# Kernel tuning notes

Measured on AMD Instinct MI355X. Metric: run time of the kernel, lower is better.

Reference implementation:

```python
import jax, jax.numpy as jnp
import numpy as np
import math

B, S, H = 2, 4096, 768
NH, HD = 12, 64  # num heads, head dim


def setup_inputs() -> dict:
    key = jax.random.key(0)
    ks = jax.random.split(key, 4)
    scale = 1.0 / math.sqrt(H)
    return {
        "hidden_states": jax.random.normal(ks[0], (B, S, H), jnp.float32),
        "attention_mask": jnp.zeros((B, 1, 1, S), jnp.float32),
        "Wq": jax.random.normal(ks[1], (H, H), jnp.float32) * scale,
        "bq": jnp.zeros((H,), jnp.float32),
        "Wk": jax.random.normal(ks[2], (H, H), jnp.float32) * scale,
        "bk": jnp.zeros((H,), jnp.float32),
        "Wv": jax.random.normal(ks[3], (H, H), jnp.float32) * scale,
        "bv": jnp.zeros((H,), jnp.float32),
    }


def reference(hidden_states, attention_mask, Wq, bq, Wk, bk, Wv, bv):
    # Linear projections (torch nn.Linear: x @ W.T + b)
    q = hidden_states @ Wq.T + bq  # [B,S,H]
    k = hidden_states @ Wk.T + bk
    v = hidden_states @ Wv.T + bv
    # split heads -> [B, NH, S, HD]
    def split(x):
        return x.reshape(B, S, NH, HD).transpose(0, 2, 1, 3)
    qh, kh, vh = split(q), split(k), split(v)
    scores = jnp.einsum('bhqd,bhkd->bhqk', qh, kh) / math.sqrt(HD)
    scores = scores + attention_mask  # additive mask, broadcast
    probs = jax.nn.softmax(scores, axis=-1)
    # dropout prob = 0.0 (inference) -> identity
    ctx = jnp.einsum('bhqk,bhkd->bhqd', probs, vh)
    ctx = ctx.transpose(0, 2, 1, 3).reshape(B, S, H)
    return ctx
```

## Files before the change

### kernel.cpp

```cpp
#include <hip/hip_runtime.h>
#include <hip/hip_bf16.h>

typedef float f32x4 __attribute__((ext_vector_type(4)));
typedef float f32x16 __attribute__((ext_vector_type(16)));
typedef short short8 __attribute__((ext_vector_type(8)));

#define LOG2E 1.44269504088896340736f

__device__ __forceinline__ ushort f2bf(float f){
  unsigned u = __builtin_bit_cast(unsigned, f);
  u = (u + 0x7fffu + ((u >> 16) & 1u)) >> 16;
  return (ushort)u;
}

__device__ __forceinline__ float exp2_hw(float x){
  float r; asm("v_exp_f32 %0, %1" : "=v"(r) : "v"(x)); return r;
}

__device__ __forceinline__ double pk_add(double a, double b){
  double d; asm("v_pk_add_f32 %0, %1, %2" : "=v"(d) : "v"(a), "v"(b)); return d;
}
__device__ __forceinline__ double pk_mul(double a, double b){
  double d; asm("v_pk_mul_f32 %0, %1, %2" : "=v"(d) : "v"(a), "v"(b)); return d;
}
__device__ __forceinline__ uint cvtpk_bf16(float lo, float hi){
  uint r; asm("v_cvt_pk_bf16_f32 %0, %1, %2" : "=v"(r) : "v"(lo), "v"(hi)); return r;
}
__device__ __forceinline__ double f2d(float x, float y){
  union { float f[2]; double d; } u; u.f[0] = x; u.f[1] = y; return u.d;
}
__device__ __forceinline__ float fmax3(float a, float b, float c){
  return fmaxf(fmaxf(a, b), c);
}

union F16u { f32x16 v; double d[8]; float f[16]; };

__global__ void cvt_kernel(const float* __restrict__ src, ushort* __restrict__ dst, int n4){
  int i = blockIdx.x * 256 + threadIdx.x;
  if (i < n4){
    float4 v = ((const float4*)src)[i];
    ushort4 o; o.x = f2bf(v.x); o.y = f2bf(v.y); o.z = f2bf(v.z); o.w = f2bf(v.w);
    ((ushort4*)dst)[i] = o;
  }
}

__global__ void scale_kernel(const float* __restrict__ src, float* __restrict__ dst,
                             float sc, int n){
  int i = blockIdx.x * 256 + threadIdx.x;
  if (i < n) dst[i] = src[i] * sc;
}

__global__ __launch_bounds__(256) void qkv_gemm(const ushort* __restrict__ Xb,
                                                const ushort* __restrict__ Wb,
                                                const float* __restrict__ bias,
                                                ushort* __restrict__ Out,
                                                float scale){
  __shared__ ushort Xs[128*64];
  __shared__ ushort Ws[128*64];
  const int m0 = blockIdx.x * 128, n0 = blockIdx.y * 128;
  const int tid = threadIdx.x, w = tid >> 6, lane = tid & 63;
  const int r = lane & 15, g = lane >> 4;
  const int wr = (w >> 1) * 64, wc = (w & 1) * 64;
  const int lrow = lane >> 3;
  const int gk = (lane & 7) ^ lrow;
  f32x4 acc[4][4] = {};
  for (int k0 = 0; k0 < 768; k0 += 64){
    #pragma unroll
    for (int p = 0; p < 4; p++){
      int rowb = p*32 + w*8;
      int row = rowb + lrow;
      __builtin_amdgcn_global_load_lds(
        (const uint4*)(Xb + (size_t)(m0+row)*768 + k0 + gk*8),
        (uint4*)((char*)Xs + rowb*128), 16, 0, 0);
      __builtin_amdgcn_global_load_lds(
        (const uint4*)(Wb + (size_t)(n0+row)*768 + k0 + gk*8),
        (uint4*)((char*)Ws + rowb*128), 16, 0, 0);
    }
    __syncthreads();
    #pragma unroll
    for (int ks = 0; ks < 2; ks++){
      short8 af[4], bf[4];
      int bo = ks*64 + g*16;
      #pragma unroll
      for (int i = 0; i < 4; i++){
        int rowa = wr + i*16 + r;
        af[i] = *(const short8*)((char*)Xs + rowa*128 + (bo ^ ((rowa&7)<<4)));
        int rowb2 = wc + i*16 + r;
        bf[i] = *(const short8*)((char*)Ws + rowb2*128 + (bo ^ ((rowb2&7)<<4)));
      }
      #pragma unroll
      for (int i = 0; i < 4; i++)
        #pragma unroll
        for (int j = 0; j < 4; j++)
          acc[i][j] = __builtin_amdgcn_mfma_f32_16x16x32_bf16(af[i], bf[j], acc[i][j], 0,0,0);
    }
    __syncthreads();
  }
  #pragma unroll
  for (int i = 0; i < 4; i++){
    #pragma unroll
    for (int j = 0; j < 4; j++){
      int col = n0 + wc + j*16 + r;
      float bv = bias[col];
      int rowb = m0 + wr + i*16 + g*4;
      #pragma unroll
      for (int q = 0; q < 4; q++)
        Out[(size_t)(rowb+q)*768 + col] = f2bf((acc[i][j][q] + bv) * scale);
    }
  }
}

__global__ __launch_bounds__(256) void qkv_gemm_vt(const ushort* __restrict__ Xb,
                                                   const ushort* __restrict__ Wb,
                                                   const float* __restrict__ bias,
                                                   ushort* __restrict__ VtOut){
  __shared__ ushort Xs[128*64];
  __shared__ ushort Ws[128*64];
  const int m0 = blockIdx.x * 128, n0 = blockIdx.y * 128;
  const int tid = threadIdx.x, w = tid >> 6, lane = tid & 63;
  const int r = lane & 15, g = lane >> 4;
  const int wr = (w >> 1) * 64, wc = (w & 1) * 64;
  const int lrow = lane >> 3;
  const int gk = (lane & 7) ^ lrow;
  f32x4 acc[4][4] = {};
  for (int k0 = 0; k0 < 768; k0 += 64){
    #pragma unroll
    for (int p = 0; p < 4; p++){
      int rowb = p*32 + w*8;
      int row = rowb + lrow;
      __builtin_amdgcn_global_load_lds(
        (const uint4*)(Xb + (size_t)(m0+row)*768 + k0 + gk*8),
        (uint4*)((char*)Xs + rowb*128), 16, 0, 0);
      __builtin_amdgcn_global_load_lds(
        (const uint4*)(Wb + (size_t)(n0+row)*768 + k0 + gk*8),
        (uint4*)((char*)Ws + rowb*128), 16, 0, 0);
    }
    __syncthreads();
    #pragma unroll
    for (int ks = 0; ks < 2; ks++){
      short8 af[4], bf[4];
      int bo = ks*64 + g*16;
      #pragma unroll
      for (int i = 0; i < 4; i++){
        int rowa = wr + i*16 + r;
        af[i] = *(const short8*)((char*)Xs + rowa*128 + (bo ^ ((rowa&7)<<4)));
        int rowb2 = wc + i*16 + r;
        bf[i] = *(const short8*)((char*)Ws + rowb2*128 + (bo ^ ((rowb2&7)<<4)));
      }
      #pragma unroll
      for (int i = 0; i < 4; i++)
        #pragma unroll
        for (int j = 0; j < 4; j++)
          acc[i][j] = __builtin_amdgcn_mfma_f32_16x16x32_bf16(af[i], bf[j], acc[i][j], 0,0,0);
    }
    __syncthreads();
  }
  #pragma unroll
  for (int i = 0; i < 4; i++){
    #pragma unroll
    for (int j = 0; j < 4; j++){
      int col = n0 + wc + j*16 + r;
      float bv = bias[col];
      int rowb = m0 + wr + i*16 + g*4;
      ushort4 o;
      o.x = f2bf(acc[i][j][0] + bv);
      o.y = f2bf(acc[i][j][1] + bv);
      o.z = f2bf(acc[i][j][2] + bv);
      o.w = f2bf(acc[i][j][3] + bv);
      size_t vrow = (size_t)((rowb >> 12) * 768 + col);
      *(ushort4*)(VtOut + vrow * 4096 + (rowb & 4095)) = o;
    }
  }
}

__global__ __launch_bounds__(256, 3) void flash_attn(const ushort* __restrict__ Qb,
                                                     const ushort* __restrict__ Kb,
                                                     const ushort* __restrict__ Vt,
                                                     const float* __restrict__ maskL,
                                                     float* __restrict__ out){
  __shared__ ushort SM[16384];
  const int tid = threadIdx.x, w = tid >> 6, lane = tid & 63;
  const int q = lane & 31, hi = lane >> 5;
  const int swq = (q & 7) << 4;
  const int h = blockIdx.y, b = blockIdx.z;
  const int q0 = blockIdx.x * 128 + w * 32;
  char* sm = (char*)SM;

  short8 bq[4];
  {
    const ushort* qp = Qb + (size_t)(b*4096 + q0 + q)*768 + h*64 + hi*8;
    #pragma unroll
    for (int kd = 0; kd < 4; kd++) bq[kd] = *(const short8*)(qp + 16*kd);
  }
  const ushort* Kbase = Kb + (size_t)(b*4096)*768 + h*64;
  const ushort* Vbase = Vt + (size_t)(b*768 + h*64)*4096;

  const int row0 = tid >> 3, cir = tid & 7;
  const int row1 = row0 + 32;
  const int wb0 = row0*128 + ((cir*16) ^ ((row0&7)<<4));
  const int wb1 = row1*128 + ((cir*16) ^ ((row1&7)<<4));
  const ushort* kp0 = Kbase + (size_t)row0*768 + cir*8;
  const ushort* kp1 = Kbase + (size_t)row1*768 + cir*8;
  const ushort* vp0 = Vbase + (size_t)row0*4096 + cir*8;
  const ushort* vp1 = Vbase + (size_t)row1*4096 + cir*8;

  int off8[8];
  #pragma unroll
  for (int s = 0; s < 2; s++)
    #pragma unroll
    for (int kd = 0; kd < 4; kd++)
      off8[s*4+kd] = (s*32 + q)*128 + ((32*kd + 16*hi) ^ swq);

  uint4 k0r = *(const uint4*)kp0, k1r = *(const uint4*)kp1;
  uint4 v0r = *(const uint4*)vp0, v1r = *(const uint4*)vp1;
  *(uint4*)(sm + wb0) = k0r;           *(uint4*)(sm + wb1) = k1r;
  *(uint4*)(sm + 16384 + wb0) = v0r;   *(uint4*)(sm + 16384 + wb1) = v1r;
  k0r = *(const uint4*)(kp0 + (size_t)64*768);
  k1r = *(const uint4*)(kp1 + (size_t)64*768);
  v0r = *(const uint4*)(vp0 + 64);
  v1r = *(const uint4*)(vp1 + 64);
  __syncthreads();

  F16u c0, c1;
  { f32x16 zz = {}; c0.v = zz; c1.v = zz; }
  float mrun = -1e30f, lrun = 0.f;

  for (int t = 0; t < 64; t++){
    const int tb = (t & 1) << 13;
    const char* kb = sm + tb;
    const char* vb = kb + 16384;
    __builtin_amdgcn_s_setprio(1);
    f32x16 z0 = {}, z1 = {};
    #pragma unroll
    for (int kd = 0; kd < 4; kd++){
      short8 ak = *(const short8*)(kb + off8[kd]);
      z0 = __builtin_amdgcn_mfma_f32_32x32x16_bf16(ak, bq[kd], z0, 0,0,0);
    }
    #pragma unroll
    for (int kd = 0; kd < 4; kd++){
      short8 ak = *(const short8*)(kb + off8[4+kd]);
      z1 = __builtin_amdgcn_mfma_f32_32x32x16_bf16(ak, bq[kd], z1, 0,0,0);
    }
    __builtin_amdgcn_s_setprio(0);
    F16u s0, s1; s0.v = z0; s1.v = z1;
    if (t < 63){
      char* wbuf = sm + (tb ^ 8192);
      *(uint4*)(wbuf + wb0) = k0r;           *(uint4*)(wbuf + wb1) = k1r;
      *(uint4*)(wbuf + 16384 + wb0) = v0r;   *(uint4*)(wbuf + 16384 + wb1) = v1r;
    }
    if (t < 62){
      const size_t kn = (size_t)(t+2) * 64;
      k0r = *(const uint4*)(kp0 + kn*768);
      k1r = *(const uint4*)(kp1 + kn*768);
      v0r = *(const uint4*)(vp0 + kn);
      v1r = *(const uint4*)(vp1 + kn);
    }
    const float* mrow = maskL + b*4096 + t*64 + hi*4;
    #pragma unroll
    for (int eq = 0; eq < 4; eq++){
      float4 m0v = *(const float4*)(mrow + eq*8);
      s0.d[2*eq]   = pk_add(s0.d[2*eq],   f2d(m0v.x, m0v.y));
      s0.d[2*eq+1] = pk_add(s0.d[2*eq+1], f2d(m0v.z, m0v.w));
      float4 m1v = *(const float4*)(mrow + 32 + eq*8);
      s1.d[2*eq]   = pk_add(s1.d[2*eq],   f2d(m1v.x, m1v.y));
      s1.d[2*eq+1] = pk_add(s1.d[2*eq+1], f2d(m1v.z, m1v.w));
    }
    float ma = fmax3(s0.f[0], s0.f[1], s0.f[2]);
    float mb = fmax3(s0.f[3], s0.f[4], s0.f[5]);
    ma = fmax3(ma, s0.f[6], s0.f[7]);
    mb = fmax3(mb, s0.f[8], s0.f[9]);
    ma = fmax3(ma, s0.f[10], s0.f[11]);
    mb = fmax3(mb, s0.f[12], s0.f[13]);
    ma = fmax3(ma, s0.f[14], s0.f[15]);
    mb = fmax3(mb, s1.f[0], s1.f[1]);
    ma = fmax3(ma, s1.f[2], s1.f[3]);
    mb = fmax3(mb, s1.f[4], s1.f[5]);
    ma = fmax3(ma, s1.f[6], s1.f[7]);
    mb = fmax3(mb, s1.f[8], s1.f[9]);
    ma = fmax3(ma, s1.f[10], s1.f[11]);
    mb = fmax3(mb, s1.f[12], s1.f[13]);
    float mt = fmax3(ma, s1.f[14], fmaxf(mb, s1.f[15]));
    mt = fmaxf(mt, __shfl_xor(mt, 32, 64));
    if (!__all(mt <= mrun + 11.5415603f)){
      float mnew = fmaxf(mrun, mt);
      float alpha = exp2_hw(mrun - mnew);
      mrun = mnew;
      lrun *= alpha;
      double al2 = f2d(alpha, alpha);
      #pragma unroll
      for (int i = 0; i < 8; i++){
        c0.d[i] = pk_mul(c0.d[i], al2);
        c1.d[i] = pk_mul(c1.d[i], al2);
      }
    }
    double msub = f2d(-mrun, -mrun);
    #pragma unroll
    for (int i = 0; i < 8; i++){
      s0.d[i] = pk_add(s0.d[i], msub);
      s1.d[i] = pk_add(s1.d[i], msub);
    }
    #pragma unroll
    for (int e = 0; e < 16; e++){
      s0.f[e] = exp2_hw(s0.f[e]);
      s1.f[e] = exp2_hw(s1.f[e]);
    }
    double t00 = pk_add(s0.d[0], s0.d[1]), t01 = pk_add(s0.d[2], s0.d[3]);
    double t02 = pk_add(s0.d[4], s0.d[5]), t03 = pk_add(s0.d[6], s0.d[7]);
    double t10 = pk_add(s1.d[0], s1.d[1]), t11 = pk_add(s1.d[2], s1.d[3]);
    double t12 = pk_add(s1.d[4], s1.d[5]), t13 = pk_add(s1.d[6], s1.d[7]);
    double u0 = pk_add(t00, t01), u1 = pk_add(t02, t03);
    double u2 = pk_add(t10, t11), u3 = pk_add(t12, t13);
    double wsum = pk_add(pk_add(u0, u1), pk_add(u2, u3));
    {
      union { double d; float f[2]; } uw; uw.d = wsum;
      float rs = uw.f[0] + uw.f[1];
      rs += __shfl_xor(rs, 32, 64);
      lrun += rs;
    }
    short8 bp[4];
    {
      uint pw[8];
      #pragma unroll
      for (int u = 0; u < 8; u++) pw[u] = cvtpk_bf16(s0.f[2*u], s0.f[2*u+1]);
      #pragma unroll
      for (int u2 = 0; u2 < 2; u2++){
        uint x0 = pw[4*u2+0], x1 = pw[4*u2+1], x2 = pw[4*u2+2], x3 = pw[4*u2+3];
        asm("v_permlane32_swap_b32 %0, %1" : "+v"(x0), "+v"(x2));
        asm("v_permlane32_swap_b32 %0, %1" : "+v"(x1), "+v"(x3));
        union { uint u[4]; short8 v; } bb;
        bb.u[0] = x0; bb.u[1] = x1; bb.u[2] = x2; bb.u[3] = x3;
        bp[u2] = bb.v;
      }
      #pragma unroll
      for (int u = 0; u < 8; u++) pw[u] = cvtpk_bf16(s1.f[2*u], s1.f[2*u+1]);
      #pragma unroll
      for (int u2 = 0; u2 < 2; u2++){
        uint x0 = pw[4*u2+0], x1 = pw[4*u2+1], x2 = pw[4*u2+2], x3 = pw[4*u2+3];
        asm("v_permlane32_swap_b32 %0, %1" : "+v"(x0), "+v"(x2));
        asm("v_permlane32_swap_b32 %0, %1" : "+v"(x1), "+v"(x3));
        union { uint u[4]; short8 v; } bb;
        bb.u[0] = x0; bb.u[1] = x1; bb.u[2] = x2; bb.u[3] = x3;
        bp[2+u2] = bb.v;
      }
    }
    __builtin_amdgcn_s_setprio(1);
    #pragma unroll
    for (int kk = 0; kk < 4; kk++){
      short8 av = *(const short8*)(vb + off8[kk]);
      c0.v = __builtin_amdgcn_mfma_f32_32x32x16_bf16(av, bp[kk], c0.v, 0,0,0);
    }
    #pragma unroll
    for (int kk = 0; kk < 4; kk++){
      short8 av = *(const short8*)(vb + off8[4+kk]);
      c1.v = __builtin_amdgcn_mfma_f32_32x32x16_bf16(av, bp[kk], c1.v, 0,0,0);
    }
    __builtin_amdgcn_s_setprio(0);
    __syncthreads();
  }
  float inv = 1.0f / lrun;
  size_t orow = (size_t)(b*4096 + q0 + q) * 768 + h*64;
  #pragma unroll
  for (int eq = 0; eq < 4; eq++){
    float4 o;
    o.x = c0.f[4*eq+0] * inv; o.y = c0.f[4*eq+1] * inv;
    o.z = c0.f[4*eq+2] * inv; o.w = c0.f[4*eq+3] * inv;
    *(float4*)(out + orow + eq*8 + hi*4) = o;
  }
  #pragma unroll
  for (int eq = 0; eq < 4; eq++){
    float4 o;
    o.x = c1.f[4*eq+0] * inv; o.y = c1.f[4*eq+1] * inv;
    o.z = c1.f[4*eq+2] * inv; o.w = c1.f[4*eq+3] * inv;
    *(float4*)(out + orow + 32 + eq*8 + hi*4) = o;
  }
}

extern "C" void kernel_launch(void* const* d_in, const int* in_sizes, int n_in,
                              void* d_out, int out_size, void* d_ws, size_t ws_size,
                              hipStream_t stream){
  const float* hidden = (const float*)d_in[0];
  const float* mask   = (const float*)d_in[1];
  const float* Wq     = (const float*)d_in[2];
  const float* bq     = (const float*)d_in[3];
  const float* Wk     = (const float*)d_in[4];
  const float* bk     = (const float*)d_in[5];
  const float* Wv     = (const float*)d_in[6];
  const float* bv     = (const float*)d_in[7];
  char* ws = (char*)d_ws;
  ushort* Xb    = (ushort*)(ws);
  ushort* Wqb   = (ushort*)(ws + 12582912);
  ushort* Wkb   = (ushort*)(ws + 13762560);
  ushort* Wvb   = (ushort*)(ws + 14942208);
  ushort* Qb    = (ushort*)(ws + 16121856);
  ushort* Kb    = (ushort*)(ws + 28704768);
  ushort* Vtb   = (ushort*)(ws + 41287680);
  float*  maskL = (float*)(ws + 53870592);

  cvt_kernel<<<6144, 256, 0, stream>>>(hidden, Xb, 1572864);
  cvt_kernel<<<576, 256, 0, stream>>>(Wq, Wqb, 147456);
  cvt_kernel<<<576, 256, 0, stream>>>(Wk, Wkb, 147456);
  cvt_kernel<<<576, 256, 0, stream>>>(Wv, Wvb, 147456);
  scale_kernel<<<32, 256, 0, stream>>>(mask, maskL, LOG2E, 8192);

  dim3 gg(64, 6);
  qkv_gemm<<<gg, 256, 0, stream>>>(Xb, Wqb, bq, Qb, 0.125f * LOG2E);
  qkv_gemm<<<gg, 256, 0, stream>>>(Xb, Wkb, bk, Kb, 1.0f);
  qkv_gemm_vt<<<gg, 256, 0, stream>>>(Xb, Wvb, bv, Vtb);

  dim3 ga(32, 12, 2);
  flash_attn<<<ga, 256, 0, stream>>>(Qb, Kb, Vtb, maskL, (float*)d_out);
}
```

Before: 231.1 us.

## Software-pipeline QK^T one tile ahead so it overlaps softmax and PV

Restructures the flash-attention loop so the QK^T MFMAs for tile t+1 are issued in the same iteration as the softmax and PV work for tile t. K now runs one tile further ahead than V, with a prologue that computes the first score tile, and the final iteration skips its barrier. The aim is to overlap the softmax VALU work with matrix-core work and hide LDS latency. It costs extra live registers for the next tile's scores and makes the K/V buffer indexing more intricate.

```diff
diff --git a/kernel.cpp b/kernel.cpp
--- a/kernel.cpp
+++ b/kernel.cpp
@@ -204,12 +204,10 @@
   const ushort* vp0 = Vbase + (size_t)row0*4096 + cir*8;
   const ushort* vp1 = Vbase + (size_t)row1*4096 + cir*8;
 
-  int off8[8];
+  int off4[4];
   #pragma unroll
-  for (int s = 0; s < 2; s++)
-    #pragma unroll
-    for (int kd = 0; kd < 4; kd++)
-      off8[s*4+kd] = (s*32 + q)*128 + ((32*kd + 16*hi) ^ swq);
+  for (int kd = 0; kd < 4; kd++)
+    off4[kd] = q*128 + ((32*kd + 16*hi) ^ swq);
 
   uint4 k0r = *(const uint4*)kp0, k1r = *(const uint4*)kp1;
   uint4 v0r = *(const uint4*)vp0, v1r = *(const uint4*)vp1;
@@ -217,6 +215,9 @@
   *(uint4*)(sm + 16384 + wb0) = v0r;   *(uint4*)(sm + 16384 + wb1) = v1r;
   k0r = *(const uint4*)(kp0 + (size_t)64*768);
   k1r = *(const uint4*)(kp1 + (size_t)64*768);
+  *(uint4*)(sm + 8192 + wb0) = k0r;    *(uint4*)(sm + 8192 + wb1) = k1r;
+  k0r = *(const uint4*)(kp0 + (size_t)128*768);
+  k1r = *(const uint4*)(kp1 + (size_t)128*768);
   v0r = *(const uint4*)(vp0 + 64);
   v1r = *(const uint4*)(vp1 + 64);
   __syncthreads();
@@ -225,35 +226,58 @@
   { f32x16 zz = {}; c0.v = zz; c1.v = zz; }
   float mrun = -1e30f, lrun = 0.f;
 
+  F16u s0, s1;
+  {
+    f32x16 z0 = {}, z1 = {};
+    #pragma unroll
+    for (int kd = 0; kd < 4; kd++){
+      short8 ak = *(const short8*)(sm + off4[kd]);
+      z0 = __builtin_amdgcn_mfma_f32_32x32x16_bf16(ak, bq[kd], z0, 0,0,0);
+    }
+    #pragma unroll
+    for (int kd = 0; kd < 4; kd++){
+      short8 ak = *(const short8*)(sm + 4096 + off4[kd]);
+      z1 = __builtin_amdgcn_mfma_f32_32x32x16_bf16(ak, bq[kd], z1, 0,0,0);
+    }
+    s0.v = z0; s1.v = z1;
+  }
+  __syncthreads();
+
   for (int t = 0; t < 64; t++){
-    const int tb = (t & 1) << 13;
-    const char* kb = sm + tb;
-    const char* vb = kb + 16384;
-    __builtin_amdgcn_s_setprio(1);
-    f32x16 z0 = {}, z1 = {};
-    #pragma unroll
-    for (int kd = 0; kd < 4; kd++){
-      short8 ak = *(const short8*)(kb + off8[kd]);
-      z0 = __builtin_amdgcn_mfma_f32_32x32x16_bf16(ak, bq[kd], z0, 0,0,0);
-    }
-    #pragma unroll
-    for (int kd = 0; kd < 4; kd++){
-      short8 ak = *(const short8*)(kb + off8[4+kd]);
-      z1 = __builtin_amdgcn_mfma_f32_32x32x16_bf16(ak, bq[kd], z1, 0,0,0);
-    }
-    __builtin_amdgcn_s_setprio(0);
-    F16u s0, s1; s0.v = z0; s1.v = z1;
+    const int tb  = (t & 1) << 13;
+    const int tbn = tb ^ 8192;
+    if (t < 62){
+      *(uint4*)(sm + tb + wb0) = k0r;
+      *(uint4*)(sm + tb + wb1) = k1r;
+    }
     if (t < 63){
-      char* wbuf = sm + (tb ^ 8192);
-      *(uint4*)(wbuf + wb0) = k0r;           *(uint4*)(wbuf + wb1) = k1r;
-      *(uint4*)(wbuf + 16384 + wb0) = v0r;   *(uint4*)(wbuf + 16384 + wb1) = v1r;
-    }
-    if (t < 62){
-      const size_t kn = (size_t)(t+2) * 64;
+      *(uint4*)(sm + 16384 + tbn + wb0) = v0r;
+      *(uint4*)(sm + 16384 + tbn + wb1) = v1r;
+    }
+    if (t < 61){
+      const size_t kn = (size_t)(t+3) * 64;
       k0r = *(const uint4*)(kp0 + kn*768);
       k1r = *(const uint4*)(kp1 + kn*768);
-      v0r = *(const uint4*)(vp0 + kn);
-      v1r = *(const uint4*)(vp1 + kn);
+    }
+    if (t < 62){
+      const size_t vn = (size_t)(t+2) * 64;
+      v0r = *(const uint4*)(vp0 + vn);
+      v1r = *(const uint4*)(vp1 + vn);
+    }
+    f32x16 z0 = {}, z1 = {};
+    if (t < 63){
+      __builtin_amdgcn_s_setprio(1);
+      #pragma unroll
+      for (int kd = 0; kd < 4; kd++){
+        short8 ak = *(const short8*)(sm + tbn + off4[kd]);
+        z0 = __builtin_amdgcn_mfma_f32_32x32x16_bf16(ak, bq[kd], z0, 0,0,0);
+      }
+      #pragma unroll
+      for (int kd = 0; kd < 4; kd++){
+        short8 ak = *(const short8*)(sm + tbn + 4096 + off4[kd]);
+        z1 = __builtin_amdgcn_mfma_f32_32x32x16_bf16(ak, bq[kd], z1, 0,0,0);
+      }
+      __builtin_amdgcn_s_setprio(0);
     }
     const float* mrow = maskL + b*4096 + t*64 + hi*4;
     #pragma unroll
@@ -346,16 +370,17 @@
     __builtin_amdgcn_s_setprio(1);
     #pragma unroll
     for (int kk = 0; kk < 4; kk++){
-      short8 av = *(const short8*)(vb + off8[kk]);
+      short8 av = *(const short8*)(sm + 16384 + tb + off4[kk]);
       c0.v = __builtin_amdgcn_mfma_f32_32x32x16_bf16(av, bp[kk], c0.v, 0,0,0);
     }
     #pragma unroll
     for (int kk = 0; kk < 4; kk++){
-      short8 av = *(const short8*)(vb + off8[4+kk]);
+      short8 av = *(const short8*)(sm + 16384 + tb + 4096 + off4[kk]);
       c1.v = __builtin_amdgcn_mfma_f32_32x32x16_bf16(av, bp[kk], c1.v, 0,0,0);
     }
     __builtin_amdgcn_s_setprio(0);
-    __syncthreads();
+    if (t < 63) __syncthreads();
+    s0.v = z0; s1.v = z1;
   }
   float inv = 1.0f / lrun;
   size_t orow = (size_t)(b*4096 + q0 + q) * 768 + h*64;
```

Result: slower. 240.5 us (+4.1%).

## Split attention key range across two blocks and merge partials

Applied to the files above, without the earlier changes.

Each attention block now processes half of the key sequence, doubling the grid, and writes unnormalized partial outputs plus running max and sum. A new merge kernel combines the two halves with log-sum-exp rescaling and normalizes. This is meant to raise parallelism and balance load across CUs. It costs extra global traffic for the partial buffers and an additional kernel launch.

```diff
diff --git a/kernel.cpp b/kernel.cpp
--- a/kernel.cpp
+++ b/kernel.cpp
@@ -177,14 +177,17 @@
                                                      const ushort* __restrict__ Kb,
                                                      const ushort* __restrict__ Vt,
                                                      const float* __restrict__ maskL,
-                                                     float* __restrict__ out){
-  __shared__ ushort SM[16384];
+                                                     float* __restrict__ part0,
+                                                     float* __restrict__ part1,
+                                                     float2* __restrict__ lm){
+  __shared__ ushort SMEM[16384];
   const int tid = threadIdx.x, w = tid >> 6, lane = tid & 63;
   const int q = lane & 31, hi = lane >> 5;
   const int swq = (q & 7) << 4;
   const int h = blockIdx.y, b = blockIdx.z;
-  const int q0 = blockIdx.x * 128 + w * 32;
-  char* sm = (char*)SM;
+  const int qt = blockIdx.x >> 1, half = blockIdx.x & 1;
+  const int q0 = qt * 128 + w * 32;
+  char* sm = (char*)SMEM;
 
   short8 bq[4];
   {
@@ -192,8 +195,8 @@
     #pragma unroll
     for (int kd = 0; kd < 4; kd++) bq[kd] = *(const short8*)(qp + 16*kd);
   }
-  const ushort* Kbase = Kb + (size_t)(b*4096)*768 + h*64;
-  const ushort* Vbase = Vt + (size_t)(b*768 + h*64)*4096;
+  const ushort* Kbase = Kb + (size_t)(b*4096 + half*2048)*768 + h*64;
+  const ushort* Vbase = Vt + (size_t)(b*768 + h*64)*4096 + half*2048;
 
   const int row0 = tid >> 3, cir = tid & 7;
   const int row1 = row0 + 32;
@@ -204,12 +207,10 @@
   const ushort* vp0 = Vbase + (size_t)row0*4096 + cir*8;
   const ushort* vp1 = Vbase + (size_t)row1*4096 + cir*8;
 
-  int off8[8];
+  int off4[4];
   #pragma unroll
-  for (int s = 0; s < 2; s++)
-    #pragma unroll
-    for (int kd = 0; kd < 4; kd++)
-      off8[s*4+kd] = (s*32 + q)*128 + ((32*kd + 16*hi) ^ swq);
+  for (int kd = 0; kd < 4; kd++)
+    off4[kd] = q*128 + ((32*kd + 16*hi) ^ swq);
 
   uint4 k0r = *(const uint4*)kp0, k1r = *(const uint4*)kp1;
   uint4 v0r = *(const uint4*)vp0, v1r = *(const uint4*)vp1;
@@ -225,7 +226,7 @@
   { f32x16 zz = {}; c0.v = zz; c1.v = zz; }
   float mrun = -1e30f, lrun = 0.f;
 
-  for (int t = 0; t < 64; t++){
+  for (int t = 0; t < 32; t++){
     const int tb = (t & 1) << 13;
     const char* kb = sm + tb;
     const char* vb = kb + 16384;
@@ -233,29 +234,29 @@
     f32x16 z0 = {}, z1 = {};
     #pragma unroll
     for (int kd = 0; kd < 4; kd++){
-      short8 ak = *(const short8*)(kb + off8[kd]);
+      short8 ak = *(const short8*)(kb + off4[kd]);
       z0 = __builtin_amdgcn_mfma_f32_32x32x16_bf16(ak, bq[kd], z0, 0,0,0);
     }
     #pragma unroll
     for (int kd = 0; kd < 4; kd++){
-      short8 ak = *(const short8*)(kb + off8[4+kd]);
+      short8 ak = *(const short8*)(kb + 4096 + off4[kd]);
       z1 = __builtin_amdgcn_mfma_f32_32x32x16_bf16(ak, bq[kd], z1, 0,0,0);
     }
     __builtin_amdgcn_s_setprio(0);
     F16u s0, s1; s0.v = z0; s1.v = z1;
-    if (t < 63){
+    if (t < 31){
       char* wbuf = sm + (tb ^ 8192);
       *(uint4*)(wbuf + wb0) = k0r;           *(uint4*)(wbuf + wb1) = k1r;
       *(uint4*)(wbuf + 16384 + wb0) = v0r;   *(uint4*)(wbuf + 16384 + wb1) = v1r;
     }
-    if (t < 62){
+    if (t < 30){
       const size_t kn = (size_t)(t+2) * 64;
       k0r = *(const uint4*)(kp0 + kn*768);
       k1r = *(const uint4*)(kp1 + kn*768);
       v0r = *(const uint4*)(vp0 + kn);
       v1r = *(const uint4*)(vp1 + kn);
     }
-    const float* mrow = maskL + b*4096 + t*64 + hi*4;
+    const float* mrow = maskL + b*4096 + half*2048 + t*64 + hi*4;
     #pragma unroll
     for (int eq = 0; eq < 4; eq++){
       float4 m0v = *(const float4*)(mrow + eq*8);
@@ -346,33 +347,63 @@
     __builtin_amdgcn_s_setprio(1);
     #pragma unroll
     for (int kk = 0; kk < 4; kk++){
-      short8 av = *(const short8*)(vb + off8[kk]);
+      short8 av = *(const short8*)(vb + off4[kk]);
       c0.v = __builtin_amdgcn_mfma_f32_32x32x16_bf16(av, bp[kk], c0.v, 0,0,0);
     }
     #pragma unroll
     for (int kk = 0; kk < 4; kk++){
-      short8 av = *(const short8*)(vb + off8[4+kk]);
+      short8 av = *(const short8*)(vb + 4096 + off4[kk]);
       c1.v = __builtin_amdgcn_mfma_f32_32x32x16_bf16(av, bp[kk], c1.v, 0,0,0);
     }
     __builtin_amdgcn_s_setprio(0);
     __syncthreads();
   }
-  float inv = 1.0f / lrun;
+  float* part = half ? part1 : part0;
   size_t orow = (size_t)(b*4096 + q0 + q) * 768 + h*64;
   #pragma unroll
   for (int eq = 0; eq < 4; eq++){
     float4 o;
-    o.x = c0.f[4*eq+0] * inv; o.y = c0.f[4*eq+1] * inv;
-    o.z = c0.f[4*eq+2] * inv; o.w = c0.f[4*eq+3] * inv;
-    *(float4*)(out + orow + eq*8 + hi*4) = o;
+    o.x = c0.f[4*eq+0]; o.y = c0.f[4*eq+1];
+    o.z = c0.f[4*eq+2]; o.w = c0.f[4*eq+3];
+    *(float4*)(part + orow + eq*8 + hi*4) = o;
   }
   #pragma unroll
   for (int eq = 0; eq < 4; eq++){
     float4 o;
-    o.x = c1.f[4*eq+0] * inv; o.y = c1.f[4*eq+1] * inv;
-    o.z = c1.f[4*eq+2] * inv; o.w = c1.f[4*eq+3] * inv;
-    *(float4*)(out + orow + 32 + eq*8 + hi*4) = o;
-  }
+    o.x = c1.f[4*eq+0]; o.y = c1.f[4*eq+1];
+    o.z = c1.f[4*eq+2]; o.w = c1.f[4*eq+3];
+    *(float4*)(part + orow + 32 + eq*8 + hi*4) = o;
+  }
+  if (hi == 0){
+    int idx = ((half*2 + b)*12 + h)*4096 + (q0 + q);
+    lm[idx] = make_float2(mrun, lrun);
+  }
+}
+
+__global__ void merge_kernel(float* __restrict__ c0, const float* __restrict__ c1,
+                             const float2* __restrict__ lm){
+  int i = blockIdx.x * 256 + threadIdx.x;
+  const int nf4 = 2*4096*768/4;
+  if (i >= nf4) return;
+  int f = i * 4;
+  int b = f / (4096*768);
+  int rem = f - b*(4096*768);
+  int qrow = rem / 768;
+  int col = rem - qrow*768;
+  int head = col >> 6;
+  float2 L0 = lm[((    b)*12 + head)*4096 + qrow];
+  float2 L1 = lm[((2 + b)*12 + head)*4096 + qrow];
+  float M = fmaxf(L0.x, L1.x);
+  float e0 = exp2f(L0.x - M), e1 = exp2f(L1.x - M);
+  float inv = 1.0f / (L0.y*e0 + L1.y*e1);
+  float4 a = ((const float4*)c0)[i];
+  float4 bb = ((const float4*)c1)[i];
+  float4 o;
+  o.x = (a.x*e0 + bb.x*e1) * inv;
+  o.y = (a.y*e0 + bb.y*e1) * inv;
+  o.z = (a.z*e0 + bb.z*e1) * inv;
+  o.w = (a.w*e0 + bb.w*e1) * inv;
+  ((float4*)c0)[i] = o;
 }
 
 extern "C" void kernel_launch(void* const* d_in, const int* in_sizes, int n_in,
@@ -395,6 +426,8 @@
   ushort* Kb    = (ushort*)(ws + 28704768);
   ushort* Vtb   = (ushort*)(ws + 41287680);
   float*  maskL = (float*)(ws + 53870592);
+  float*  part1 = (float*)(ws + 53903360);
+  float2* lmbuf = (float2*)(ws + 79069184);
 
   cvt_kernel<<<6144, 256, 0, stream>>>(hidden, Xb, 1572864);
   cvt_kernel<<<576, 256, 0, stream>>>(Wq, Wqb, 147456);
@@ -407,6 +440,8 @@
   qkv_gemm<<<gg, 256, 0, stream>>>(Xb, Wkb, bk, Kb, 1.0f);
   qkv_gemm_vt<<<gg, 256, 0, stream>>>(Xb, Wvb, bv, Vtb);
 
-  dim3 ga(32, 12, 2);
-  flash_attn<<<ga, 256, 0, stream>>>(Qb, Kb, Vtb, maskL, (float*)d_out);
-}
+  dim3 ga(64, 12, 2);
+  flash_attn<<<ga, 256, 0, stream>>>(Qb, Kb, Vtb, maskL,
+                                     (float*)d_out, part1, lmbuf);
+  merge_kernel<<<6144, 256, 0, stream>>>((float*)d_out, part1, lmbuf);
+}
```

Result: no change. 234.9 us (+1.7%).
